# Optimization experiments

Measured on AMD Instinct MI355X. Metric: run time of the kernel, lower is better.

## Reference

```python
import jax, jax.numpy as jnp
import numpy as np

BANDS = [[0,63],[48,111],[96,159],[144,207],[192,255],[240,303],[288,351],[336,399],[384,447],[432,495],[480,543],[528,591],[576,639],[624,687],[672,735],[720,783],[768,831],[816,879],[864,927],[912,975],[960,1023],[961,1024]]
N_FFT, WIN, HOP, FREQ = 2048, 2048, 512, 1025
B, T, D = 8, 2048, 128
NB = len(BANDS)
WIDTH = BANDS[0][1] - BANDS[0][0] + 1  # 64, all bands equal width
STARTS = np.array([s for s, _ in BANDS])
POS = STARTS[:, None] + np.arange(WIDTH)[None, :]  # (NB, WIDTH) freq-bin indices


def setup_inputs() -> dict:
    key = jax.random.key(0)
    k1, k2, k3 = jax.random.split(key, 3)
    z = jax.random.normal(k1, (B, T, NB, D), jnp.float32)
    mix_spec = jax.random.normal(k2, (B, 2, T, FREQ), jnp.float32)
    W = jax.random.normal(k3, (NB, D, WIDTH * 2), jnp.float32) * 1e-4  # init std=0.0001
    b = jnp.zeros((NB, WIDTH * 2), jnp.float32).at[:, 0::2].set(1.0)   # real part bias = 1
    return {"z": z, "mix_spec": mix_spec, "W": W, "b": b}


def _istft(spec_r, spec_i):
    # spec_r/spec_i: (B, T, F) -> waveform (B, HOP*(T-1)), center=True semantics
    comp = spec_r + 1j * spec_i
    frames = jnp.fft.irfft(comp, n=N_FFT, axis=-1)  # (B, T, n_fft)
    n = jnp.arange(WIN, dtype=frames.dtype)
    win = 0.5 * (1.0 - jnp.cos(2.0 * jnp.pi * n / WIN))  # periodic Hann
    frames = frames * win
    total = HOP * (T - 1) + N_FFT
    pos = HOP * jnp.arange(T)[:, None] + jnp.arange(N_FFT)[None, :]  # (T, n_fft)
    out = jnp.zeros((frames.shape[0], total), frames.dtype).at[:, pos].add(frames)
    env = jnp.zeros((total,), frames.dtype).at[pos].add(win * win)
    out = out / jnp.where(env > 1e-11, env, 1.0)
    start = N_FFT // 2
    return out[:, start:start + HOP * (T - 1)]


def reference(z, mix_spec, W, b):
    # per-band linear projections (all same width -> one batched einsum)
    band = jnp.einsum('btnd,ndo->btno', z, W) + b          # (B, T, NB, 2*WIDTH)
    band = band.reshape(B, T, NB, WIDTH, 2)
    # scatter-add into overlapping frequency ranges + overlap-count normalization
    mask = jnp.zeros((B, T, FREQ, 2), z.dtype).at[:, :, POS, :].add(band)
    wgt = jnp.zeros((FREQ,), z.dtype).at[POS].add(1.0)
    mask = mask / jnp.maximum(wgt, 1.0)[None, None, :, None]
    mask_r, mask_i = mask[..., 0], mask[..., 1]            # (B, T, F)
    mix_r, mix_i = mix_spec[:, 0], mix_spec[:, 1]          # (B, T, F)
    out_r = mask_r * mix_r - mask_i * mix_i
    out_i = mask_r * mix_i + mask_i * mix_r
    return _istft(out_r, out_i)
```

## Files before the change

### kernel.cpp

```cpp
#include <hip/hip_runtime.h>

typedef _Float16 f16x8 __attribute__((ext_vector_type(8)));
typedef _Float16 f16x2 __attribute__((ext_vector_type(2)));
typedef float f32x4 __attribute__((ext_vector_type(4)));

#define SLOT_DW 2048
#define WT_BYTE_OFF 134217728
#define PHYS(i) ((i) + ((i) >> 5))

__device__ float4 d_TW4[5][256];
__device__ float2 d_TW2[5][256];
__device__ float2 d_PK[513];
__device__ float2 d_WN2[1024];
__device__ float4 d_GL[1025];

__device__ __forceinline__ void async_copy16(const void* g, void* l) {
  __builtin_amdgcn_global_load_lds((const __attribute__((address_space(1))) void*)g,
                                   (__attribute__((address_space(3))) void*)l, 16, 0, 0);
}

__global__ __launch_bounds__(256) void k_init(const float* __restrict__ W,
                                              _Float16* __restrict__ Wt) {
  int n = blockIdx.x >> 2, dq = blockIdx.x & 3;
  int tid = threadIdx.x;
  __shared__ _Float16 L[32 * 130];
  const float* Wn = W + (size_t)n * 16384 + dq * 32 * 128;
  for (int el = tid; el < 4096; el += 256) {
    int dl = el >> 7, o = el & 127;
    L[dl * 130 + o] = (_Float16)(Wn[el] * 4096.0f);
  }
  __syncthreads();
  _Float16* Wtn = Wt + (size_t)n * 16384 + dq * 32;
  for (int el = tid; el < 4096; el += 256) {
    int o = el >> 5, dl = el & 31;
    Wtn[o * 128 + dl] = L[dl * 130 + o];
  }
}

__global__ __launch_bounds__(256) void k_tab(const float* __restrict__ bias) {
  int i = blockIdx.x * 256 + threadIdx.x;
  if (i < 1280) {
    int st = i >> 8, tid = i & 255;
    int s = 2 * st;
    int qm = (tid >> s) << s;
    float ang = (float)qm * 6.135923151542565e-3f;
    d_TW4[st][tid] = make_float4(cosf(ang), sinf(ang), cosf(2.0f * ang), sinf(2.0f * ang));
    d_TW2[st][tid] = make_float2(cosf(3.0f * ang), sinf(3.0f * ang));
  } else if (i < 1280 + 1025) {
    int f = i - 1280;
    int nhi = f / 48; if (nhi > 20) nhi = 20;
    int nlo = (f >= 16) ? (f - 16) / 48 : 0;
    int cnt = nhi - nlo + 1;
    int has21 = (f >= 961) ? 1 : 0;
    float bsr = 0.f, bsi = 0.f;
    for (int n = nlo; n <= nhi; n++) {
      bsr += bias[32 * n + 2 * f];
      bsi += bias[32 * n + 2 * f + 1];
    }
    if (has21) { bsr += bias[766 + 2 * f]; bsi += bias[766 + 2 * f + 1]; }
    int wgt = cnt + has21;
    float inv = 1.0f / (float)wgt;
    d_GL[f] = make_float4(0.0f, inv, bsr * inv, bsi * inv);
  } else if (i < 1280 + 1025 + 513) {
    int k = i - 2305;
    float ang = (float)k * 3.0679615757712823e-3f;
    d_PK[k] = make_float2(cosf(ang), sinf(ang));
  } else if (i < 1280 + 1025 + 513 + 1024) {
    int j = i - 2818;
    const float inv_n = 1.0f / 2048.0f;
    float w0 = inv_n * 0.5f * (1.0f - cosf((float)(2 * j)     * 3.0679615757712823e-3f));
    float w1 = inv_n * 0.5f * (1.0f - cosf((float)(2 * j + 1) * 3.0679615757712823e-3f));
    d_WN2[j] = make_float2(w0, w1);
  }
}

__global__ __launch_bounds__(256) void kA(const float* __restrict__ z,
                                          const _Float16* __restrict__ Wt,
                                          _Float16* __restrict__ band) {
  int mt = blockIdx.x;
  int n  = blockIdx.y;
  int r0 = mt * 64;
  __shared__ __align__(16) char smem[33280];
  int tid = threadIdx.x;
  int lane = tid & 63, wave = tid >> 6;
  int l16 = lane & 15, quad = lane >> 4;

  const _Float16* Wn = Wt + (size_t)n * 16384;
  f16x8 bfrag[8];
#pragma unroll
  for (int kb = 0; kb < 4; kb++) {
    int ko = kb * 32 + quad * 8;
    bfrag[2 * kb]     = *(const f16x8*)(Wn + (wave * 32 + l16) * 128 + ko);
    bfrag[2 * kb + 1] = *(const f16x8*)(Wn + (wave * 32 + 16 + l16) * 128 + ko);
  }

  {
    int col16 = lane & 31;
    int rowh  = lane >> 5;
#pragma unroll
    for (int it = 0; it < 8; it++) {
      int pr = wave * 8 + it;
      const float* g = z + ((size_t)(r0 + 2 * pr + rowh) * 22 + n) * 128 + col16 * 4;
      async_copy16(g, smem + pr * 1040);
    }
  }
  __syncthreads();

  f32x4 acc[2][4];
#pragma unroll
  for (int c = 0; c < 2; c++)
#pragma unroll
    for (int rt = 0; rt < 4; rt++) acc[c][rt] = (f32x4){0.f, 0.f, 0.f, 0.f};

#pragma unroll
  for (int kb = 0; kb < 4; kb++) {
#pragma unroll
    for (int rt = 0; rt < 4; rt++) {
      int row = rt * 16 + l16;
      const float* ap = (const float*)(smem + (row >> 1) * 1040 + (row & 1) * 512) + kb * 32 + quad * 8;
      float4 v0 = *(const float4*)ap;
      float4 v1 = *(const float4*)(ap + 4);
      f16x8 a;
      a[0] = (_Float16)v0.x; a[1] = (_Float16)v0.y; a[2] = (_Float16)v0.z; a[3] = (_Float16)v0.w;
      a[4] = (_Float16)v1.x; a[5] = (_Float16)v1.y; a[6] = (_Float16)v1.z; a[7] = (_Float16)v1.w;
      acc[0][rt] = __builtin_amdgcn_mfma_f32_16x16x32_f16(a, bfrag[2 * kb],     acc[0][rt], 0, 0, 0);
      acc[1][rt] = __builtin_amdgcn_mfma_f32_16x16x32_f16(a, bfrag[2 * kb + 1], acc[1][rt], 0, 0, 0);
    }
  }
  __syncthreads();

  _Float16* Cs = (_Float16*)smem;
  const float inv_scale = 1.0f / 4096.0f;
#pragma unroll
  for (int c = 0; c < 2; c++) {
    int col = (wave * 2 + c) * 16 + l16;
#pragma unroll
    for (int rt = 0; rt < 4; rt++) {
#pragma unroll
      for (int reg = 0; reg < 4; reg++) {
        int row = rt * 16 + quad * 4 + reg;
        Cs[row * 136 + col] = (_Float16)(acc[c][rt][reg] * inv_scale);
      }
    }
  }
  __syncthreads();
  int row = tid >> 2;
  int c4 = (tid & 3) * 32;
  const _Float16* srcl = &Cs[row * 136 + c4];
  _Float16* dst = band + (size_t)(r0 + row) * (SLOT_DW * 2) + n * 128 + c4;
  f16x8 v0 = *(const f16x8*)(srcl);
  f16x8 v1 = *(const f16x8*)(srcl + 8);
  f16x8 v2 = *(const f16x8*)(srcl + 16);
  f16x8 v3 = *(const f16x8*)(srcl + 24);
  *(f16x8*)(dst)      = v0;
  *(f16x8*)(dst + 8)  = v1;
  *(f16x8*)(dst + 16) = v2;
  *(f16x8*)(dst + 24) = v3;
}


#define GLOAD(S, F) \
  int nhi##S = (F) / 48; if (nhi##S > 20) nhi##S = 20; \
  int nlo##S = ((F) >= 16) ? ((F) - 16) / 48 : 0; \
  int cnt##S = nhi##S - nlo##S + 1; \
  int bas##S = 32 * nlo##S + 2 * (F); \
  f16x2 v0##S = *(const f16x2*)(bandg + bas##S); \
  f16x2 v1##S = *(const f16x2*)(bandg + bas##S + (cnt##S > 1 ? 32 : 0)); \
  f16x2 v2##S = *(const f16x2*)(bandg + (((F) >= 961) ? (766 + 2 * (F)) : bas##S));

#define GCOMB(S, F, GE, XR, XI, OR_, OI_) { \
  float c0 = (cnt##S >= 1) ? 1.f : 0.f; \
  float c1 = (cnt##S > 1) ? 1.f : 0.f; \
  float c2 = ((F) >= 961) ? 1.f : 0.f; \
  float sr = c0 * (float)(v0##S[0]) + c1 * (float)(v1##S[0]) + c2 * (float)(v2##S[0]); \
  float si = c0 * (float)(v0##S[1]) + c1 * (float)(v1##S[1]) + c2 * (float)(v2##S[1]); \
  float mr = sr * (GE).y + (GE).z; \
  float mi = si * (GE).y + (GE).w; \
  OR_ = mr * (XR) - mi * (XI); \
  OI_ = mr * (XI) + mi * (XR); }

__global__ __launch_bounds__(256) void kB(const float* __restrict__ mix,
                                          float* __restrict__ ws) {
  int r = blockIdx.x;
  int b = r >> 11, t = r & 2047;
  __shared__ __align__(16) float2 bufA[1056];
  __shared__ __align__(16) float2 bufB[1056];
  int tid = threadIdx.x;

  const _Float16* bandg = (const _Float16*)(ws + (size_t)r * SLOT_DW);
  const float* mixr = mix + ((size_t)(b * 2) * 2048 + t) * 1025;
  const float* mixi = mix + ((size_t)(b * 2 + 1) * 2048 + t) * 1025;

  int f00 = tid, f01 = 1024 - tid, f10 = tid + 256, f11 = 768 - tid;

  float4 nw4 = d_TW4[0][tid];
  float2 nw2 = d_TW2[0][tid];
  float4 gl00 = d_GL[f00], gl01 = d_GL[f01], gl10 = d_GL[f10], gl11 = d_GL[f11];
  float4 gle  = d_GL[512];
  float2 pk0 = d_PK[tid], pk1 = d_PK[tid + 256];
  GLOAD(a, f00) GLOAD(b, f01) GLOAD(c, f10) GLOAD(d, f11) GLOAD(e, 512)
  float xr00 = mixr[f00], xi00 = mixi[f00];
  float xr01 = mixr[f01], xi01 = mixi[f01];
  float xr10 = mixr[f10], xi10 = mixi[f10];
  float xr11 = mixr[f11], xi11 = mixi[f11];
  float xre  = mixr[512], xie  = mixi[512];

  float X00r, X00i, X01r, X01i, X10r, X10i, X11r, X11i, Xer, Xei;
  GCOMB(a, f00, gl00, xr00, xi00, X00r, X00i);
  GCOMB(b, f01, gl01, xr01, xi01, X01r, X01i);
  GCOMB(c, f10, gl10, xr10, xi10, X10r, X10i);
  GCOMB(d, f11, gl11, xr11, xi11, X11r, X11i);
  GCOMB(e, 512, gle,  xre,  xie,  Xer,  Xei);
  if (tid == 0) { X00i = 0.0f; X01i = 0.0f; }

  {
    float Ar = X00r + X01r, Ai = X00i - X01i;
    float Br = X00r - X01r, Bi = X00i + X01i;
    float s1 = pk0.x * Bi + pk0.y * Br;
    float s2 = pk0.x * Br - pk0.y * Bi;
    bufA[PHYS(tid)] = make_float2(Ar - s1, Ai + s2);
    if (tid > 0) bufA[PHYS(1024 - tid)] = make_float2(Ar + s1, -Ai + s2);
  }
  {
    float Ar = X10r + X11r, Ai = X10i - X11i;
    float Br = X10r - X11r, Bi = X10i + X11i;
    float s1 = pk1.x * Bi + pk1.y * Br;
    float s2 = pk1.x * Br - pk1.y * Bi;
    bufA[PHYS(tid + 256)] = make_float2(Ar - s1, Ai + s2);
    bufA[PHYS(768 - tid)] = make_float2(Ar + s1, -Ai + s2);
  }
  if (tid == 0) bufA[PHYS(512)] = make_float2(2.0f * Xer, -2.0f * Xei);

  float2* src = bufA;
  float2* dst = bufB;
  float2 wnA, wnB, wnC, wnD;
#pragma unroll
  for (int st = 0; st < 4; st++) {
    const int s = 2 * st;
    const int m = 1 << s;
    float wc1 = nw4.x, ws1 = nw4.y, wc2 = nw4.z, ws2 = nw4.w;
    float wc3 = nw2.x, ws3 = nw2.y;
    if (st < 3) {
      nw4 = d_TW4[st + 1][tid];
      nw2 = d_TW2[st + 1][tid];
    } else {
      wnA = d_WN2[tid];
      wnB = d_WN2[tid + 256];
      wnC = d_WN2[tid + 512];
      wnD = d_WN2[tid + 768];
    }
    __syncthreads();
    int q = tid >> s, rr = tid & (m - 1);
    float2 x0 = src[PHYS(tid)];
    float2 x1 = src[PHYS(tid + 256)];
    float2 x2 = src[PHYS(tid + 512)];
    float2 x3 = src[PHYS(tid + 768)];
    float tAr = x0.x + x2.x, tAi = x0.y + x2.y;
    float tBr = x0.x - x2.x, tBi = x0.y - x2.y;
    float tCr = x1.x + x3.x, tCi = x1.y + x3.y;
    float tDr = x1.x - x3.x, tDi = x1.y - x3.y;
    int base = 4 * q * m + rr;
    dst[PHYS(base)] = make_float2(tAr + tCr, tAi + tCi);
    float pr = tBr - tDi, pi = tBi + tDr;
    dst[PHYS(base + m)] = make_float2(wc1 * pr - ws1 * pi, wc1 * pi + ws1 * pr);
    float qr = tAr - tCr, qi = tAi - tCi;
    dst[PHYS(base + 2 * m)] = make_float2(wc2 * qr - ws2 * qi, wc2 * qi + ws2 * qr);
    float rr2 = tBr + tDi, ri2 = tBi - tDr;
    dst[PHYS(base + 3 * m)] = make_float2(wc3 * rr2 - ws3 * ri2, wc3 * ri2 + ws3 * rr2);
    float2* tmp = src; src = dst; dst = tmp;
  }
  __syncthreads();

  {
    float2 x0 = src[PHYS(tid)];
    float2 x1 = src[PHYS(tid + 256)];
    float2 x2 = src[PHYS(tid + 512)];
    float2 x3 = src[PHYS(tid + 768)];
    float tAr = x0.x + x2.x, tAi = x0.y + x2.y;
    float tBr = x0.x - x2.x, tBi = x0.y - x2.y;
    float tCr = x1.x + x3.x, tCi = x1.y + x3.y;
    float tDr = x1.x - x3.x, tDi = x1.y - x3.y;
    float2* slot2 = (float2*)(ws + (size_t)r * SLOT_DW);
    slot2[tid]       = make_float2((tAr + tCr) * wnA.x, (tAi + tCi) * wnA.y);
    slot2[tid + 256] = make_float2((tBr - tDi) * wnB.x, (tBi + tDr) * wnB.y);
    slot2[tid + 512] = make_float2((tAr - tCr) * wnC.x, (tAi - tCi) * wnC.y);
    slot2[tid + 768] = make_float2((tBr + tDi) * wnD.x, (tBi - tDr) * wnD.y);
  }
}

__global__ __launch_bounds__(256) void kC(const float* __restrict__ ws,
                                          float* __restrict__ out) {
  int b = blockIdx.y;
  int g = blockIdx.x * 256 + threadIdx.x;
  if (g >= 262016) return;
  int p = g * 4;
  int q = p + 1024;
  int t1 = q >> 9;          if (t1 > 2047) t1 = 2047;
  int t0 = (q - 1536) >> 9; if (t0 < 0) t0 = 0;
  const float* base = ws + (size_t)b * 2048 * SLOT_DW;
  float s0 = 0.f, s1 = 0.f, s2 = 0.f, s3 = 0.f;
  for (int t = t0; t <= t1; t++) {
    int i = q - (t << 9);
    float4 v = *(const float4*)(base + (size_t)t * SLOT_DW + i);
    s0 += v.x; s1 += v.y; s2 += v.z; s3 += v.w;
  }
  float4 res;
  if (t1 - t0 == 3) {
    const float inv_env = 0.66666666667f;
    res = make_float4(s0 * inv_env, s1 * inv_env, s2 * inv_env, s3 * inv_env);
  } else {
    float env[4] = {0.f, 0.f, 0.f, 0.f};
    for (int t = t0; t <= t1; t++) {
      int i0 = q - (t << 9);
#pragma unroll
      for (int e = 0; e < 4; e++) {
        float c = __cosf((float)(i0 + e) * 3.0679615757712823e-3f);
        float w = 0.5f * (1.0f - c);
        env[e] += w * w;
      }
    }
#pragma unroll
    for (int e = 0; e < 4; e++) env[e] = (env[e] > 1e-11f) ? env[e] : 1.0f;
    res = make_float4(s0 / env[0], s1 / env[1], s2 / env[2], s3 / env[3]);
  }
  *(float4*)(out + (size_t)b * 1048064 + p) = res;
}

extern "C" void kernel_launch(void* const* d_in, const int* in_sizes, int n_in,
                              void* d_out, int out_size, void* d_ws, size_t ws_size,
                              hipStream_t stream) {
  const float* z    = (const float*)d_in[0];
  const float* mix  = (const float*)d_in[1];
  const float* W    = (const float*)d_in[2];
  const float* bias = (const float*)d_in[3];
  float* out = (float*)d_out;
  _Float16* Wt = (_Float16*)((char*)d_ws + WT_BYTE_OFF);

  k_init<<<88, 256, 0, stream>>>(W, Wt);
  k_tab<<<16, 256, 0, stream>>>(bias);
  kA<<<dim3(256, 22), 256, 0, stream>>>(z, Wt, (_Float16*)d_ws);
  kB<<<16384, 256, 0, stream>>>(mix, (float*)d_ws);
  kC<<<dim3(1024, 8), 256, 0, stream>>>((const float*)d_ws, out);
}
```

Baseline: 478.6 us.

## Swizzle FFT LDS indexing, merge init kernels, widen overlap-add to 8 outputs

Replaces the padded LDS index mapping in the FFT kernel with an XOR swizzle, which shrinks the shared buffers from 1056 to 1024 entries and aims to avoid bank conflicts without padding. Merges the weight-transpose and table-setup kernels into one launch to save a launch. The overlap-add kernel now makes each thread produce 8 outputs using two float4 loads per frame, halving the thread count. The interior path is fully unrolled over its four frames. Risks include a swizzle that does not remove conflicts for every access stride and higher register use in the overlap-add kernel.

```diff
diff --git a/kernel.cpp b/kernel.cpp
--- a/kernel.cpp
+++ b/kernel.cpp
@@ -6,7 +6,7 @@
 
 #define SLOT_DW 2048
 #define WT_BYTE_OFF 134217728
-#define PHYS(i) ((i) + ((i) >> 5))
+#define PHYS(i) ((i) ^ (((i) >> 4) & 3) ^ ((((i) >> 6) & 3) << 2))
 
 __device__ float4 d_TW4[5][256];
 __device__ float2 d_TW2[5][256];
@@ -20,32 +20,33 @@
 }
 
 __global__ __launch_bounds__(256) void k_init(const float* __restrict__ W,
-                                              _Float16* __restrict__ Wt) {
-  int n = blockIdx.x >> 2, dq = blockIdx.x & 3;
+                                              _Float16* __restrict__ Wt,
+                                              const float* __restrict__ bias) {
   int tid = threadIdx.x;
-  __shared__ _Float16 L[32 * 130];
-  const float* Wn = W + (size_t)n * 16384 + dq * 32 * 128;
-  for (int el = tid; el < 4096; el += 256) {
-    int dl = el >> 7, o = el & 127;
-    L[dl * 130 + o] = (_Float16)(Wn[el] * 4096.0f);
-  }
-  __syncthreads();
-  _Float16* Wtn = Wt + (size_t)n * 16384 + dq * 32;
-  for (int el = tid; el < 4096; el += 256) {
-    int o = el >> 5, dl = el & 31;
-    Wtn[o * 128 + dl] = L[dl * 130 + o];
-  }
-}
-
-__global__ __launch_bounds__(256) void k_tab(const float* __restrict__ bias) {
-  int i = blockIdx.x * 256 + threadIdx.x;
+  if (blockIdx.x < 88) {
+    int n = blockIdx.x >> 2, dq = blockIdx.x & 3;
+    __shared__ _Float16 L[32 * 130];
+    const float* Wn = W + (size_t)n * 16384 + dq * 32 * 128;
+    for (int el = tid; el < 4096; el += 256) {
+      int dl = el >> 7, o = el & 127;
+      L[dl * 130 + o] = (_Float16)(Wn[el] * 4096.0f);
+    }
+    __syncthreads();
+    _Float16* Wtn = Wt + (size_t)n * 16384 + dq * 32;
+    for (int el = tid; el < 4096; el += 256) {
+      int o = el >> 5, dl = el & 31;
+      Wtn[o * 128 + dl] = L[dl * 130 + o];
+    }
+    return;
+  }
+  int i = (blockIdx.x - 88) * 256 + tid;
   if (i < 1280) {
-    int st = i >> 8, tid = i & 255;
+    int st = i >> 8, t = i & 255;
     int s = 2 * st;
-    int qm = (tid >> s) << s;
+    int qm = (t >> s) << s;
     float ang = (float)qm * 6.135923151542565e-3f;
-    d_TW4[st][tid] = make_float4(cosf(ang), sinf(ang), cosf(2.0f * ang), sinf(2.0f * ang));
-    d_TW2[st][tid] = make_float2(cosf(3.0f * ang), sinf(3.0f * ang));
+    d_TW4[st][t] = make_float4(cosf(ang), sinf(ang), cosf(2.0f * ang), sinf(2.0f * ang));
+    d_TW2[st][t] = make_float2(cosf(3.0f * ang), sinf(3.0f * ang));
   } else if (i < 1280 + 1025) {
     int f = i - 1280;
     int nhi = f / 48; if (nhi > 20) nhi = 20;
@@ -183,8 +184,8 @@
                                           float* __restrict__ ws) {
   int r = blockIdx.x;
   int b = r >> 11, t = r & 2047;
-  __shared__ __align__(16) float2 bufA[1056];
-  __shared__ __align__(16) float2 bufB[1056];
+  __shared__ __align__(16) float2 bufA[1024];
+  __shared__ __align__(16) float2 bufB[1024];
   int tid = threadIdx.x;
 
   const _Float16* bandg = (const _Float16*)(ws + (size_t)r * SLOT_DW);
@@ -292,38 +293,53 @@
                                           float* __restrict__ out) {
   int b = blockIdx.y;
   int g = blockIdx.x * 256 + threadIdx.x;
-  if (g >= 262016) return;
-  int p = g * 4;
+  if (g >= 131008) return;
+  int p = g * 8;
   int q = p + 1024;
   int t1 = q >> 9;          if (t1 > 2047) t1 = 2047;
   int t0 = (q - 1536) >> 9; if (t0 < 0) t0 = 0;
   const float* base = ws + (size_t)b * 2048 * SLOT_DW;
-  float s0 = 0.f, s1 = 0.f, s2 = 0.f, s3 = 0.f;
-  for (int t = t0; t <= t1; t++) {
-    int i = q - (t << 9);
-    float4 v = *(const float4*)(base + (size_t)t * SLOT_DW + i);
-    s0 += v.x; s1 += v.y; s2 += v.z; s3 += v.w;
-  }
-  float4 res;
+  float s[8] = {0.f, 0.f, 0.f, 0.f, 0.f, 0.f, 0.f, 0.f};
   if (t1 - t0 == 3) {
+#pragma unroll
+    for (int e = 0; e < 4; e++) {
+      int tt = t0 + e;
+      int i = q - (tt << 9);
+      const float* fp = base + (size_t)tt * SLOT_DW + i;
+      float4 va = *(const float4*)(fp);
+      float4 vb = *(const float4*)(fp + 4);
+      s[0] += va.x; s[1] += va.y; s[2] += va.z; s[3] += va.w;
+      s[4] += vb.x; s[5] += vb.y; s[6] += vb.z; s[7] += vb.w;
+    }
     const float inv_env = 0.66666666667f;
-    res = make_float4(s0 * inv_env, s1 * inv_env, s2 * inv_env, s3 * inv_env);
+    float4 r0 = make_float4(s[0] * inv_env, s[1] * inv_env, s[2] * inv_env, s[3] * inv_env);
+    float4 r1 = make_float4(s[4] * inv_env, s[5] * inv_env, s[6] * inv_env, s[7] * inv_env);
+    float* op = out + (size_t)b * 1048064 + p;
+    *(float4*)(op)     = r0;
+    *(float4*)(op + 4) = r1;
   } else {
-    float env[4] = {0.f, 0.f, 0.f, 0.f};
-    for (int t = t0; t <= t1; t++) {
-      int i0 = q - (t << 9);
-#pragma unroll
-      for (int e = 0; e < 4; e++) {
-        float c = __cosf((float)(i0 + e) * 3.0679615757712823e-3f);
+    float env[8] = {0.f, 0.f, 0.f, 0.f, 0.f, 0.f, 0.f, 0.f};
+    for (int tt = t0; tt <= t1; tt++) {
+      int i = q - (tt << 9);
+      const float* fp = base + (size_t)tt * SLOT_DW + i;
+      float4 va = *(const float4*)(fp);
+      float4 vb = *(const float4*)(fp + 4);
+      s[0] += va.x; s[1] += va.y; s[2] += va.z; s[3] += va.w;
+      s[4] += vb.x; s[5] += vb.y; s[6] += vb.z; s[7] += vb.w;
+#pragma unroll
+      for (int e = 0; e < 8; e++) {
+        float c = __cosf((float)(i + e) * 3.0679615757712823e-3f);
         float w = 0.5f * (1.0f - c);
         env[e] += w * w;
       }
     }
-#pragma unroll
-    for (int e = 0; e < 4; e++) env[e] = (env[e] > 1e-11f) ? env[e] : 1.0f;
-    res = make_float4(s0 / env[0], s1 / env[1], s2 / env[2], s3 / env[3]);
-  }
-  *(float4*)(out + (size_t)b * 1048064 + p) = res;
+    float* op = out + (size_t)b * 1048064 + p;
+#pragma unroll
+    for (int e = 0; e < 8; e++) {
+      float ev = (env[e] > 1e-11f) ? env[e] : 1.0f;
+      op[e] = s[e] / ev;
+    }
+  }
 }
 
 extern "C" void kernel_launch(void* const* d_in, const int* in_sizes, int n_in,
@@ -336,9 +352,8 @@
   float* out = (float*)d_out;
   _Float16* Wt = (_Float16*)((char*)d_ws + WT_BYTE_OFF);
 
-  k_init<<<88, 256, 0, stream>>>(W, Wt);
-  k_tab<<<16, 256, 0, stream>>>(bias);
+  k_init<<<104, 256, 0, stream>>>(W, Wt, bias);
   kA<<<dim3(256, 22), 256, 0, stream>>>(z, Wt, (_Float16*)d_ws);
   kB<<<16384, 256, 0, stream>>>(mix, (float*)d_ws);
-  kC<<<dim3(1024, 8), 256, 0, stream>>>((const float*)d_ws, out);
-}
+  kC<<<dim3(512, 8), 256, 0, stream>>>((const float*)d_ws, out);
+}
```

Result: no change. 475.5 us (-0.7%).
